# Optimization experiments

Measured on AMD Instinct MI355X. Metric: run time of the kernel, lower is better.

## Reference

```python
import jax, jax.numpy as jnp
import numpy as np

N_NODES = 100000
N_EDGES = 1600000
IN_DIM = 128
HID_DIM = 256
OUT_DIM = 128
K = 10
ALPHA = 0.1


def setup_inputs() -> dict:
    key = jax.random.key(0)
    k1, k2, k3, k4, k5, k6, k7 = jax.random.split(key, 7)
    feat = jax.random.normal(k1, (N_NODES, IN_DIM), dtype=jnp.float32)
    src = jax.random.randint(k2, (N_EDGES,), 0, N_NODES, dtype=jnp.int64)
    dst = jax.random.randint(k3, (N_EDGES,), 0, N_NODES, dtype=jnp.int64)
    # MLP params (Linear: y = x @ W + b), kaiming-ish scale
    W1 = jax.random.normal(k4, (IN_DIM, HID_DIM), dtype=jnp.float32) * (1.0 / np.sqrt(IN_DIM))
    b1 = jax.random.normal(k5, (HID_DIM,), dtype=jnp.float32) * 0.01
    W2 = jax.random.normal(k6, (HID_DIM, OUT_DIM), dtype=jnp.float32) * (1.0 / np.sqrt(HID_DIM))
    b2 = jax.random.normal(k7, (OUT_DIM,), dtype=jnp.float32) * 0.01
    return {"feat": feat, "W1": W1, "b1": b1, "W2": W2, "b2": b2, "src": src, "dst": dst}


def reference(feat, W1, b1, W2, b2, src, dst):
    N = feat.shape[0]
    # dgl.add_self_loop: append (i, i) for every node
    loops = jnp.arange(N, dtype=src.dtype)
    src_sl = jnp.concatenate([src, loops])
    dst_sl = jnp.concatenate([dst, loops])
    # symmetric normalization from in-degrees (with self-loops), clamped >= 1
    deg = jax.ops.segment_sum(jnp.ones_like(dst_sl, dtype=feat.dtype), dst_sl, num_segments=N)
    norm = jnp.clip(deg, 1.0) ** -0.5  # [N]

    # APPNP propagation: h <- (1-alpha) * D^-1/2 A D^-1/2 h + alpha * feat
    def hop(h, _):
        m = (h * norm[:, None])[src_sl]                      # gather scaled src feats [E+N, D]
        agg = jax.ops.segment_sum(m, dst_sl, num_segments=N)  # scatter-sum to dst [N, D]
        h = (1.0 - ALPHA) * (agg * norm[:, None]) + ALPHA * feat
        return h, None

    h, _ = jax.lax.scan(hop, feat, None, length=K)
    # 2-layer MLP: Linear -> ReLU -> Linear
    x = jax.nn.relu(h @ W1 + b1)
    return x @ W2 + b2
```

## Files before the change

kernel.cpp:

```cpp
#include <hip/hip_runtime.h>

#define IN_DIM 128
#define HID_DIM 256
#define OUT_DIM 128
#define KHOPS 10

typedef __attribute__((ext_vector_type(8))) short bf16x8;
typedef __attribute__((ext_vector_type(4))) float f32x4;

__device__ __forceinline__ unsigned short f2bf(float x) {
    unsigned int b = __float_as_uint(x);
    unsigned int r = (b + 0x7FFFu + ((b >> 16) & 1u)) >> 16;
    return (unsigned short)r;
}
__device__ __forceinline__ unsigned int pack_bf2(float lo, float hi) {
    return (unsigned int)f2bf(lo) | ((unsigned int)f2bf(hi) << 16);
}
__device__ __forceinline__ float bf_lo(unsigned int u) { return __uint_as_float(u << 16); }
__device__ __forceinline__ float bf_hi(unsigned int u) { return __uint_as_float(u & 0xFFFF0000u); }


__global__ void count_init(int* __restrict__ cnt, int* __restrict__ fill, int N) {
    int i = blockIdx.x * blockDim.x + threadIdx.x;
    if (i < N) { cnt[i] = 0; fill[i] = 0; }
}

__global__ void count_edges(const int* __restrict__ dst, int* __restrict__ cnt, int E) {
    int e = blockIdx.x * blockDim.x + threadIdx.x;
    if (e < E) atomicAdd(&cnt[dst[e]], 1);
}

__global__ void norm_kernel(const int* __restrict__ cnt, float* __restrict__ norm, int N) {
    int i = blockIdx.x * blockDim.x + threadIdx.x;
    if (i < N) {
        float deg = (float)(cnt[i] + 1);
        norm[i] = rsqrtf(deg);
    }
}

__global__ void scan_block(const int* __restrict__ cnt, int* __restrict__ row_ptr,
                           int* __restrict__ bsum, int N) {
    __shared__ int s[256];
    int tid = threadIdx.x;
    int gid = blockIdx.x * 256 + tid;
    int v = (gid < N) ? cnt[gid] : 0;
    s[tid] = v;
    __syncthreads();
    for (int off = 1; off < 256; off <<= 1) {
        int t = (tid >= off) ? s[tid - off] : 0;
        __syncthreads();
        s[tid] += t;
        __syncthreads();
    }
    if (gid < N) row_ptr[gid] = s[tid] - v;
    if (tid == 255) bsum[blockIdx.x] = s[255];
}

__global__ void scan_top(int* __restrict__ bsum, int nb) {
    __shared__ int s[512];
    int tid = threadIdx.x;
    int v = (tid < nb) ? bsum[tid] : 0;
    s[tid] = v;
    __syncthreads();
    for (int off = 1; off < 512; off <<= 1) {
        int t = (tid >= off) ? s[tid - off] : 0;
        __syncthreads();
        s[tid] += t;
        __syncthreads();
    }
    if (tid < nb) bsum[tid] = s[tid] - v;
}

__global__ void scan_add(int* __restrict__ row_ptr, const int* __restrict__ bsum,
                         int N, int E) {
    int gid = blockIdx.x * 256 + threadIdx.x;
    if (gid < N) row_ptr[gid] += bsum[blockIdx.x];
    if (gid == 0) row_ptr[N] = E;
}

__global__ void fill_csr(const int* __restrict__ src, const int* __restrict__ dst,
                         const int* __restrict__ row_ptr, int* __restrict__ fill,
                         int* __restrict__ col, int E) {
    int e = blockIdx.x * blockDim.x + threadIdx.x;
    if (e < E) {
        int d = dst[e];
        int p = atomicAdd(&fill[d], 1);
        col[row_ptr[d] + p] = src[e];
    }
}


__global__ void pack_w1(const float* __restrict__ W1, short* __restrict__ W1s) {
    int i = blockIdx.x * 256 + threadIdx.x;
    if (i >= 16 * 4 * 64 * 8) return;
    int j = i & 7, l = (i >> 3) & 63, kf = (i >> 9) & 3, rf = i >> 11;
    int k = kf * 32 + (l >> 4) * 8 + j;
    int r = rf * 16 + (l & 15);
    W1s[i] = (short)f2bf(W1[(size_t)k * HID_DIM + r]);
}

__global__ void pack_w2(const float* __restrict__ W2, short* __restrict__ W2s) {
    int i = blockIdx.x * 256 + threadIdx.x;
    if (i >= 8 * 8 * 64 * 8) return;
    int j = i & 7, l = (i >> 3) & 63, kf = (i >> 9) & 7, rf = i >> 12;
    int k = kf * 32 + (l >> 4) * 8 + j;
    int r = rf * 16 + (l & 15);
    W2s[i] = (short)f2bf(W2[(size_t)k * OUT_DIM + r]);
}


__global__ void init_g(const float* __restrict__ feat, const float* __restrict__ norm,
                       unsigned int* __restrict__ sh, unsigned int* __restrict__ ffeat,
                       int N) {
    int idx = blockIdx.x * blockDim.x + threadIdx.x;
    int total = N * 64;
    if (idx >= total) return;
    int row = idx >> 6;
    int l   = idx & 63;
    float nr = norm[row];
    float2 f = *(const float2*)(feat + (size_t)row * IN_DIM + l * 2);
    sh[idx]    = pack_bf2(nr * f.x, nr * f.y);
    ffeat[idx] = pack_bf2(0.1f * nr * f.x, 0.1f * nr * f.y);
}

__global__ __launch_bounds__(256) void hop_kernel(
    const unsigned int* __restrict__ sh_in, unsigned int* __restrict__ sh_out,
    const unsigned int* __restrict__ ffeat, const float* __restrict__ norm,
    const int* __restrict__ row_ptr, const int* __restrict__ col,
    int N) {
    int node = __builtin_amdgcn_readfirstlane(blockIdx.x * 4 + (threadIdx.x >> 6));
    int lane = threadIdx.x & 63;
    if (node >= N) return;
    size_t base = (size_t)node * 64 + lane;
    unsigned int uself = sh_in[base];
    float2 acc = { bf_lo(uself), bf_hi(uself) };
    int beg = row_ptr[node], end = row_ptr[node + 1];
    int e = beg;
    for (; e + 7 < end; e += 8) {
        int s0 = col[e],     s1 = col[e + 1], s2 = col[e + 2], s3 = col[e + 3];
        int s4 = col[e + 4], s5 = col[e + 5], s6 = col[e + 6], s7 = col[e + 7];
        unsigned int u0 = sh_in[(size_t)s0 * 64 + lane];
        unsigned int u1 = sh_in[(size_t)s1 * 64 + lane];
        unsigned int u2 = sh_in[(size_t)s2 * 64 + lane];
        unsigned int u3 = sh_in[(size_t)s3 * 64 + lane];
        unsigned int u4 = sh_in[(size_t)s4 * 64 + lane];
        unsigned int u5 = sh_in[(size_t)s5 * 64 + lane];
        unsigned int u6 = sh_in[(size_t)s6 * 64 + lane];
        unsigned int u7 = sh_in[(size_t)s7 * 64 + lane];
        acc.x += (bf_lo(u0) + bf_lo(u1)) + (bf_lo(u2) + bf_lo(u3))
               + (bf_lo(u4) + bf_lo(u5)) + (bf_lo(u6) + bf_lo(u7));
        acc.y += (bf_hi(u0) + bf_hi(u1)) + (bf_hi(u2) + bf_hi(u3))
               + (bf_hi(u4) + bf_hi(u5)) + (bf_hi(u6) + bf_hi(u7));
    }
    for (; e < end; ++e) {
        unsigned int u = sh_in[(size_t)col[e] * 64 + lane];
        acc.x += bf_lo(u);
        acc.y += bf_hi(u);
    }
    float nr = norm[node];
    float c1 = 0.9f * nr * nr;
    unsigned int uff = ffeat[base];
    float ox = c1 * acc.x + bf_lo(uff);
    float oy = c1 * acc.y + bf_hi(uff);
    sh_out[base] = pack_bf2(ox, oy);
}


#define LDA 136
#define LDH 264

__global__ __launch_bounds__(256) void mlp_mfma(
    const unsigned int* __restrict__ sh, const float* __restrict__ norm,
    const short* __restrict__ W1s, const float* __restrict__ b1,
    const short* __restrict__ W2s, const float* __restrict__ b2,
    float* __restrict__ out, int N)
{
    __shared__ short Ah[64 * LDA];
    __shared__ short Hid[64 * LDH];
    int tid  = threadIdx.x;
    int wid  = tid >> 6;
    int lane = tid & 63;
    int row0 = blockIdx.x * 64;

    for (int i = tid; i < 64 * 64; i += 256) {
        int r = i >> 6, c = i & 63;
        int row = row0 + r;
        unsigned int u = 0;
        float inv = 1.f;
        if (row < N) { u = sh[(size_t)row * 64 + c]; inv = 1.0f / norm[row]; }
        *(unsigned int*)&Ah[r * LDA + c * 2] = pack_bf2(bf_lo(u) * inv, bf_hi(u) * inv);
    }
    __syncthreads();

    int m = lane & 15;
    int g = lane >> 4;

    {
        bf16x8 Bf[4][4];
        #pragma unroll
        for (int kf = 0; kf < 4; ++kf)
            #pragma unroll
            for (int cf = 0; cf < 4; ++cf)
                Bf[kf][cf] = *(const bf16x8*)&Ah[(cf * 16 + m) * LDA + kf * 32 + g * 8];

        f32x4 acc[4][4];
        #pragma unroll
        for (int i = 0; i < 4; ++i)
            #pragma unroll
            for (int cf = 0; cf < 4; ++cf)
                acc[i][cf] = (f32x4){0.f, 0.f, 0.f, 0.f};

        #pragma unroll
        for (int i = 0; i < 4; ++i) {
            int rf = wid * 4 + i;
            #pragma unroll
            for (int kf = 0; kf < 4; ++kf) {
                bf16x8 Af = *(const bf16x8*)(W1s + (((size_t)(rf * 4 + kf)) * 64 + lane) * 8);
                #pragma unroll
                for (int cf = 0; cf < 4; ++cf)
                    acc[i][cf] = __builtin_amdgcn_mfma_f32_16x16x32_bf16(
                        Af, Bf[kf][cf], acc[i][cf], 0, 0, 0);
            }
        }

        #pragma unroll
        for (int i = 0; i < 4; ++i) {
            int feat0 = (wid * 4 + i) * 16 + g * 4;
            float4 bias = *(const float4*)(b1 + feat0);
            #pragma unroll
            for (int cf = 0; cf < 4; ++cf) {
                int node = cf * 16 + m;
                float v0 = acc[i][cf][0] + bias.x; v0 = v0 > 0.f ? v0 : 0.f;
                float v1 = acc[i][cf][1] + bias.y; v1 = v1 > 0.f ? v1 : 0.f;
                float v2 = acc[i][cf][2] + bias.z; v2 = v2 > 0.f ? v2 : 0.f;
                float v3 = acc[i][cf][3] + bias.w; v3 = v3 > 0.f ? v3 : 0.f;
                uint2 p;
                p.x = pack_bf2(v0, v1);
                p.y = pack_bf2(v2, v3);
                *(uint2*)&Hid[node * LDH + feat0] = p;
            }
        }
    }
    __syncthreads();

    {
        f32x4 acc2[2][4];
        #pragma unroll
        for (int i = 0; i < 2; ++i)
            #pragma unroll
            for (int cf = 0; cf < 4; ++cf)
                acc2[i][cf] = (f32x4){0.f, 0.f, 0.f, 0.f};

        #pragma unroll
        for (int kf = 0; kf < 8; ++kf) {
            bf16x8 Bh[4];
            #pragma unroll
            for (int cf = 0; cf < 4; ++cf)
                Bh[cf] = *(const bf16x8*)&Hid[(cf * 16 + m) * LDH + kf * 32 + g * 8];
            #pragma unroll
            for (int i = 0; i < 2; ++i) {
                int rf = wid * 2 + i;
                bf16x8 Af = *(const bf16x8*)(W2s + (((size_t)(rf * 8 + kf)) * 64 + lane) * 8);
                #pragma unroll
                for (int cf = 0; cf < 4; ++cf)
                    acc2[i][cf] = __builtin_amdgcn_mfma_f32_16x16x32_bf16(
                        Af, Bh[cf], acc2[i][cf], 0, 0, 0);
            }
        }

        #pragma unroll
        for (int i = 0; i < 2; ++i) {
            int feat0 = (wid * 2 + i) * 16 + g * 4;
            float4 bias = *(const float4*)(b2 + feat0);
            #pragma unroll
            for (int cf = 0; cf < 4; ++cf) {
                int node = row0 + cf * 16 + m;
                if (node < N) {
                    float4 o;
                    o.x = acc2[i][cf][0] + bias.x;
                    o.y = acc2[i][cf][1] + bias.y;
                    o.z = acc2[i][cf][2] + bias.z;
                    o.w = acc2[i][cf][3] + bias.w;
                    *(float4*)(out + (size_t)node * OUT_DIM + feat0) = o;
                }
            }
        }
    }
}


extern "C" void kernel_launch(void* const* d_in, const int* in_sizes, int n_in,
                              void* d_out, int out_size, void* d_ws, size_t ws_size,
                              hipStream_t stream) {
    const float* feat = (const float*)d_in[0];
    const float* W1   = (const float*)d_in[1];
    const float* b1   = (const float*)d_in[2];
    const float* W2   = (const float*)d_in[3];
    const float* b2   = (const float*)d_in[4];
    const int*   src  = (const int*)d_in[5];
    const int*   dst  = (const int*)d_in[6];
    float* out = (float*)d_out;

    int N = in_sizes[0] / IN_DIM;
    int E = in_sizes[5];

    size_t off = 0;
    auto carve = [&](size_t bytes) -> void* {
        void* p = (char*)d_ws + off;
        off += (bytes + 255) & ~(size_t)255;
        return p;
    };
    float* norm    = (float*)carve((size_t)N * 4);
    int*   cnt     = (int*)carve((size_t)N * 4);
    int*   row_ptr = (int*)carve((size_t)(N + 1) * 4);
    int*   fill    = (int*)carve((size_t)N * 4);
    int*   bsum    = (int*)carve(512 * 4);
    int*   col     = (int*)carve((size_t)E * 4);
    unsigned int* shA   = (unsigned int*)carve((size_t)N * 64 * 4);
    unsigned int* shB   = (unsigned int*)carve((size_t)N * 64 * 4);
    unsigned int* ffeat = (unsigned int*)carve((size_t)N * 64 * 4);
    short* W1s = (short*)carve((size_t)16 * 4 * 64 * 8 * 2);
    short* W2s = (short*)carve((size_t)8 * 8 * 64 * 8 * 2);
    (void)ws_size;

    int nbN = (N + 255) / 256;
    int nbE = (E + 255) / 256;

    count_init<<<nbN, 256, 0, stream>>>(cnt, fill, N);
    count_edges<<<nbE, 256, 0, stream>>>(dst, cnt, E);
    norm_kernel<<<nbN, 256, 0, stream>>>(cnt, norm, N);
    scan_block<<<nbN, 256, 0, stream>>>(cnt, row_ptr, bsum, N);
    scan_top<<<1, 512, 0, stream>>>(bsum, nbN);
    scan_add<<<nbN, 256, 0, stream>>>(row_ptr, bsum, N, E);
    fill_csr<<<nbE, 256, 0, stream>>>(src, dst, row_ptr, fill, col, E);

    pack_w1<<<128, 256, 0, stream>>>(W1, W1s);
    pack_w2<<<256, 256, 0, stream>>>(W2, W2s);

    int nbG = ((size_t)N * 64 + 255) / 256;
    init_g<<<nbG, 256, 0, stream>>>(feat, norm, shA, ffeat, N);

    int nbHop = (N + 3) / 4;
    for (int t = 0; t < KHOPS; ++t) {
        const unsigned int* si = (t % 2 == 0) ? shA : shB;
        unsigned int*       so = (t % 2 == 0) ? shB : shA;
        hop_kernel<<<nbHop, 256, 0, stream>>>(si, so, ffeat, norm, row_ptr, col, N);
    }

    int nbM = (N + 63) / 64;
    mlp_mfma<<<nbM, 256, 0, stream>>>(shA, norm, W1s, b1, W2s, b2, out, N);
}
```

Baseline: 885.7 us.

## Pre-bucket edges by destination range before CSR build

Adds a coarse radix pass that partitions edges into 32 buckets keyed by dst>>12, writing (src,dst) pairs grouped by bucket. The degree count and CSR fill then read these pairs, so their atomics and col writes hit a narrower address range per region and gain locality. The cost is an extra pass over all edges, three extra launches and an 8-byte-per-edge temporary buffer. Node ids up to 131071 fit the 32 buckets.

```diff
diff --git a/kernel.cpp b/kernel.cpp
--- a/kernel.cpp
+++ b/kernel.cpp
@@ -5,6 +5,9 @@
 #define OUT_DIM 128
 #define KHOPS 10
 
+#define NBUCK 32
+#define NBLK_B 640
+
 typedef __attribute__((ext_vector_type(8))) short bf16x8;
 typedef __attribute__((ext_vector_type(4))) float f32x4;
 
@@ -20,14 +23,61 @@
 __device__ __forceinline__ float bf_hi(unsigned int u) { return __uint_as_float(u & 0xFFFF0000u); }
 
 
-__global__ void count_init(int* __restrict__ cnt, int* __restrict__ fill, int N) {
+__global__ void count_init(int* __restrict__ cnt, int* __restrict__ fill,
+                           int* __restrict__ bucket_cnt, int N) {
     int i = blockIdx.x * blockDim.x + threadIdx.x;
     if (i < N) { cnt[i] = 0; fill[i] = 0; }
-}
-
-__global__ void count_edges(const int* __restrict__ dst, int* __restrict__ cnt, int E) {
+    if (i < NBUCK) bucket_cnt[i] = 0;
+}
+
+__global__ __launch_bounds__(256) void bucket_count(
+    const int* __restrict__ dst, int* __restrict__ bucket_cnt,
+    int* __restrict__ blk_base, int E) {
+    __shared__ int h[NBUCK];
+    int tid = threadIdx.x;
+    if (tid < NBUCK) h[tid] = 0;
+    __syncthreads();
+    for (int e = blockIdx.x * 256 + tid; e < E; e += NBLK_B * 256)
+        atomicAdd(&h[dst[e] >> 12], 1);
+    __syncthreads();
+    if (tid < NBUCK)
+        blk_base[blockIdx.x * NBUCK + tid] = atomicAdd(&bucket_cnt[tid], h[tid]);
+}
+
+__global__ void bucket_scan(const int* __restrict__ bucket_cnt,
+                            int* __restrict__ bucket_start) {
+    __shared__ int s[NBUCK];
+    int tid = threadIdx.x;
+    int v = bucket_cnt[tid];
+    s[tid] = v;
+    __syncthreads();
+    for (int off = 1; off < NBUCK; off <<= 1) {
+        int t = (tid >= off) ? s[tid - off] : 0;
+        __syncthreads();
+        s[tid] += t;
+        __syncthreads();
+    }
+    bucket_start[tid] = s[tid] - v;
+}
+
+__global__ __launch_bounds__(256) void bucket_fill(
+    const int* __restrict__ src, const int* __restrict__ dst,
+    const int* __restrict__ bucket_start, const int* __restrict__ blk_base,
+    uint2* __restrict__ pairs, int E) {
+    __shared__ int base[NBUCK];
+    int tid = threadIdx.x;
+    if (tid < NBUCK) base[tid] = bucket_start[tid] + blk_base[blockIdx.x * NBUCK + tid];
+    __syncthreads();
+    for (int e = blockIdx.x * 256 + tid; e < E; e += NBLK_B * 256) {
+        int d = dst[e], s = src[e];
+        int p = atomicAdd(&base[d >> 12], 1);
+        pairs[p] = make_uint2((unsigned)s, (unsigned)d);
+    }
+}
+
+__global__ void count_pairs(const uint2* __restrict__ pairs, int* __restrict__ cnt, int E) {
     int e = blockIdx.x * blockDim.x + threadIdx.x;
-    if (e < E) atomicAdd(&cnt[dst[e]], 1);
+    if (e < E) atomicAdd(&cnt[pairs[e].y], 1);
 }
 
 __global__ void norm_kernel(const int* __restrict__ cnt, float* __restrict__ norm, int N) {
@@ -78,14 +128,13 @@
     if (gid == 0) row_ptr[N] = E;
 }
 
-__global__ void fill_csr(const int* __restrict__ src, const int* __restrict__ dst,
-                         const int* __restrict__ row_ptr, int* __restrict__ fill,
-                         int* __restrict__ col, int E) {
+__global__ void fill_pairs(const uint2* __restrict__ pairs, const int* __restrict__ row_ptr,
+                           int* __restrict__ fill, int* __restrict__ col, int E) {
     int e = blockIdx.x * blockDim.x + threadIdx.x;
     if (e < E) {
-        int d = dst[e];
-        int p = atomicAdd(&fill[d], 1);
-        col[row_ptr[d] + p] = src[e];
+        uint2 pr = pairs[e];
+        int p = atomicAdd(&fill[pr.y], 1);
+        col[row_ptr[pr.y] + p] = (int)pr.x;
     }
 }
 
@@ -321,18 +370,25 @@
     unsigned int* ffeat = (unsigned int*)carve((size_t)N * 64 * 4);
     short* W1s = (short*)carve((size_t)16 * 4 * 64 * 8 * 2);
     short* W2s = (short*)carve((size_t)8 * 8 * 64 * 8 * 2);
+    int*   bucket_cnt   = (int*)carve(NBUCK * 4);
+    int*   bucket_start = (int*)carve(NBUCK * 4);
+    int*   blk_base     = (int*)carve((size_t)NBLK_B * NBUCK * 4);
+    uint2* pairs        = (uint2*)carve((size_t)E * 8);
     (void)ws_size;
 
     int nbN = (N + 255) / 256;
     int nbE = (E + 255) / 256;
 
-    count_init<<<nbN, 256, 0, stream>>>(cnt, fill, N);
-    count_edges<<<nbE, 256, 0, stream>>>(dst, cnt, E);
+    count_init<<<nbN, 256, 0, stream>>>(cnt, fill, bucket_cnt, N);
+    bucket_count<<<NBLK_B, 256, 0, stream>>>(dst, bucket_cnt, blk_base, E);
+    bucket_scan<<<1, NBUCK, 0, stream>>>(bucket_cnt, bucket_start);
+    bucket_fill<<<NBLK_B, 256, 0, stream>>>(src, dst, bucket_start, blk_base, pairs, E);
+    count_pairs<<<nbE, 256, 0, stream>>>(pairs, cnt, E);
     norm_kernel<<<nbN, 256, 0, stream>>>(cnt, norm, N);
     scan_block<<<nbN, 256, 0, stream>>>(cnt, row_ptr, bsum, N);
     scan_top<<<1, 512, 0, stream>>>(bsum, nbN);
     scan_add<<<nbN, 256, 0, stream>>>(row_ptr, bsum, N, E);
-    fill_csr<<<nbE, 256, 0, stream>>>(src, dst, row_ptr, fill, col, E);
+    fill_pairs<<<nbE, 256, 0, stream>>>(pairs, row_ptr, fill, col, E);
 
     pack_w1<<<128, 256, 0, stream>>>(W1, W1s);
     pack_w2<<<256, 256, 0, stream>>>(W2, W2s);
```

Result: faster. 859.6 us (-2.9%).

## Build CSR via two-level bucket sort with shared-memory histograms

Applied to the files above, without the earlier changes.

Replaces the global-atomic CSR build (count, three-kernel scan, atomic fill) with a two-pass bucket sort. Edges are first binned into 512-node buckets using per-block shared-memory histograms, then each bucket is sorted locally in LDS, which also writes row_ptr and norm. This is meant to cut scattered global atomics and the random col writes, at the cost of an extra pairs buffer and a dependence on bucket sizes fitting in LDS (with a global fallback). The packing assumes N ≤ 131072 and at most 256 buckets.

```diff
diff --git a/kernel.cpp b/kernel.cpp
--- a/kernel.cpp
+++ b/kernel.cpp
@@ -5,6 +5,10 @@
 #define OUT_DIM 128
 #define KHOPS 10
 
+#define NB2 256
+#define NBLK_B 640
+#define CAP2 12288
+
 typedef __attribute__((ext_vector_type(8))) short bf16x8;
 typedef __attribute__((ext_vector_type(4))) float f32x4;
 
@@ -20,73 +24,101 @@
 __device__ __forceinline__ float bf_hi(unsigned int u) { return __uint_as_float(u & 0xFFFF0000u); }
 
 
-__global__ void count_init(int* __restrict__ cnt, int* __restrict__ fill, int N) {
-    int i = blockIdx.x * blockDim.x + threadIdx.x;
-    if (i < N) { cnt[i] = 0; fill[i] = 0; }
-}
-
-__global__ void count_edges(const int* __restrict__ dst, int* __restrict__ cnt, int E) {
-    int e = blockIdx.x * blockDim.x + threadIdx.x;
-    if (e < E) atomicAdd(&cnt[dst[e]], 1);
-}
-
-__global__ void norm_kernel(const int* __restrict__ cnt, float* __restrict__ norm, int N) {
-    int i = blockIdx.x * blockDim.x + threadIdx.x;
-    if (i < N) {
-        float deg = (float)(cnt[i] + 1);
-        norm[i] = rsqrtf(deg);
-    }
-}
-
-__global__ void scan_block(const int* __restrict__ cnt, int* __restrict__ row_ptr,
-                           int* __restrict__ bsum, int N) {
-    __shared__ int s[256];
+__global__ void zero_buckets(int* __restrict__ bucket_cnt) {
+    if (threadIdx.x < NB2) bucket_cnt[threadIdx.x] = 0;
+}
+
+__global__ __launch_bounds__(256) void bucket_count(
+    const int* __restrict__ dst, int* __restrict__ bucket_cnt,
+    int* __restrict__ blk_base, int E) {
+    __shared__ int h[NB2];
     int tid = threadIdx.x;
-    int gid = blockIdx.x * 256 + tid;
-    int v = (gid < N) ? cnt[gid] : 0;
+    h[tid] = 0;
+    __syncthreads();
+    for (int e = blockIdx.x * 256 + tid; e < E; e += NBLK_B * 256)
+        atomicAdd(&h[dst[e] >> 9], 1);
+    __syncthreads();
+    blk_base[blockIdx.x * NB2 + tid] = atomicAdd(&bucket_cnt[tid], h[tid]);
+}
+
+__global__ void bucket_scan(const int* __restrict__ bucket_cnt,
+                            int* __restrict__ bucket_start) {
+    __shared__ int s[NB2];
+    int tid = threadIdx.x;
+    int v = bucket_cnt[tid];
     s[tid] = v;
     __syncthreads();
-    for (int off = 1; off < 256; off <<= 1) {
+    for (int off = 1; off < NB2; off <<= 1) {
         int t = (tid >= off) ? s[tid - off] : 0;
         __syncthreads();
         s[tid] += t;
         __syncthreads();
     }
-    if (gid < N) row_ptr[gid] = s[tid] - v;
-    if (tid == 255) bsum[blockIdx.x] = s[255];
-}
-
-__global__ void scan_top(int* __restrict__ bsum, int nb) {
-    __shared__ int s[512];
+    bucket_start[tid] = s[tid] - v;
+}
+
+__global__ __launch_bounds__(256) void bucket_fill(
+    const int* __restrict__ src, const int* __restrict__ dst,
+    const int* __restrict__ bucket_start, const int* __restrict__ blk_base,
+    unsigned int* __restrict__ pairs, int E) {
+    __shared__ int base[NB2];
     int tid = threadIdx.x;
-    int v = (tid < nb) ? bsum[tid] : 0;
-    s[tid] = v;
+    base[tid] = bucket_start[tid] + blk_base[blockIdx.x * NB2 + tid];
+    __syncthreads();
+    for (int e = blockIdx.x * 256 + tid; e < E; e += NBLK_B * 256) {
+        int d = dst[e], s = src[e];
+        int p = atomicAdd(&base[d >> 9], 1);
+        pairs[p] = (unsigned int)s | ((unsigned int)(d & 511) << 17);
+    }
+}
+
+__global__ __launch_bounds__(512) void build_csr(
+    const unsigned int* __restrict__ pairs, const int* __restrict__ bucket_start,
+    int* __restrict__ row_ptr, float* __restrict__ norm, int* __restrict__ col,
+    int N, int E) {
+    int bk = blockIdx.x;
+    int node0 = bk << 9;
+    int nn = min(512, N - node0);
+    int ebeg = bucket_start[bk];
+    int eend = (bk + 1 < NB2) ? bucket_start[bk + 1] : E;
+    __shared__ int hist[512];
+    __shared__ int sc[512];
+    __shared__ int lcol[CAP2];
+    int tid = threadIdx.x;
+    hist[tid] = 0;
+    __syncthreads();
+    for (int e = ebeg + tid; e < eend; e += 512)
+        atomicAdd(&hist[pairs[e] >> 17], 1);
+    __syncthreads();
+    int deg = hist[tid];
+    sc[tid] = deg;
     __syncthreads();
     for (int off = 1; off < 512; off <<= 1) {
-        int t = (tid >= off) ? s[tid - off] : 0;
+        int t = (tid >= off) ? sc[tid - off] : 0;
         __syncthreads();
-        s[tid] += t;
+        sc[tid] += t;
         __syncthreads();
     }
-    if (tid < nb) bsum[tid] = s[tid] - v;
-}
-
-__global__ void scan_add(int* __restrict__ row_ptr, const int* __restrict__ bsum,
-                         int N, int E) {
-    int gid = blockIdx.x * 256 + threadIdx.x;
-    if (gid < N) row_ptr[gid] += bsum[blockIdx.x];
-    if (gid == 0) row_ptr[N] = E;
-}
-
-__global__ void fill_csr(const int* __restrict__ src, const int* __restrict__ dst,
-                         const int* __restrict__ row_ptr, int* __restrict__ fill,
-                         int* __restrict__ col, int E) {
-    int e = blockIdx.x * blockDim.x + threadIdx.x;
-    if (e < E) {
-        int d = dst[e];
-        int p = atomicAdd(&fill[d], 1);
-        col[row_ptr[d] + p] = src[e];
-    }
+    int excl = sc[tid] - deg;
+    if (tid < nn) {
+        row_ptr[node0 + tid] = ebeg + excl;
+        norm[node0 + tid] = rsqrtf((float)(deg + 1));
+    }
+    hist[tid] = excl;
+    __syncthreads();
+    for (int e = ebeg + tid; e < eend; e += 512) {
+        unsigned int p = pairs[e];
+        int dlow = p >> 17;
+        int pos = atomicAdd(&hist[dlow], 1);
+        int s = (int)(p & 0x1FFFFu);
+        if (pos < CAP2) lcol[pos] = s;
+        else col[ebeg + pos] = s;
+    }
+    __syncthreads();
+    int tot = eend - ebeg;
+    int n_out = tot < CAP2 ? tot : CAP2;
+    for (int i = tid; i < n_out; i += 512) col[ebeg + i] = lcol[i];
+    if (bk == 0 && tid == 0) row_ptr[N] = E;
 }
 
 
@@ -311,28 +343,26 @@
         return p;
     };
     float* norm    = (float*)carve((size_t)N * 4);
-    int*   cnt     = (int*)carve((size_t)N * 4);
     int*   row_ptr = (int*)carve((size_t)(N + 1) * 4);
-    int*   fill    = (int*)carve((size_t)N * 4);
-    int*   bsum    = (int*)carve(512 * 4);
     int*   col     = (int*)carve((size_t)E * 4);
     unsigned int* shA   = (unsigned int*)carve((size_t)N * 64 * 4);
     unsigned int* shB   = (unsigned int*)carve((size_t)N * 64 * 4);
     unsigned int* ffeat = (unsigned int*)carve((size_t)N * 64 * 4);
     short* W1s = (short*)carve((size_t)16 * 4 * 64 * 8 * 2);
     short* W2s = (short*)carve((size_t)8 * 8 * 64 * 8 * 2);
+    int*   bucket_cnt   = (int*)carve(NB2 * 4);
+    int*   bucket_start = (int*)carve(NB2 * 4);
+    int*   blk_base     = (int*)carve((size_t)NBLK_B * NB2 * 4);
+    unsigned int* pairs = (unsigned int*)carve((size_t)E * 4);
     (void)ws_size;
 
-    int nbN = (N + 255) / 256;
-    int nbE = (E + 255) / 256;
-
-    count_init<<<nbN, 256, 0, stream>>>(cnt, fill, N);
-    count_edges<<<nbE, 256, 0, stream>>>(dst, cnt, E);
-    norm_kernel<<<nbN, 256, 0, stream>>>(cnt, norm, N);
-    scan_block<<<nbN, 256, 0, stream>>>(cnt, row_ptr, bsum, N);
-    scan_top<<<1, 512, 0, stream>>>(bsum, nbN);
-    scan_add<<<nbN, 256, 0, stream>>>(row_ptr, bsum, N, E);
-    fill_csr<<<nbE, 256, 0, stream>>>(src, dst, row_ptr, fill, col, E);
+    int nbBK = (N + 511) >> 9;
+
+    zero_buckets<<<1, NB2, 0, stream>>>(bucket_cnt);
+    bucket_count<<<NBLK_B, 256, 0, stream>>>(dst, bucket_cnt, blk_base, E);
+    bucket_scan<<<1, NB2, 0, stream>>>(bucket_cnt, bucket_start);
+    bucket_fill<<<NBLK_B, 256, 0, stream>>>(src, dst, bucket_start, blk_base, pairs, E);
+    build_csr<<<nbBK, 512, 0, stream>>>(pairs, bucket_start, row_ptr, norm, col, N, E);
 
     pack_w1<<<128, 256, 0, stream>>>(W1, W1s);
     pack_w2<<<256, 256, 0, stream>>>(W2, W2s);
```

New measurement: 747.6 us. 1.18x faster.
